# Kernel optimization log

Measured on AMD Instinct MI355X. Metric: run time of the kernel, lower is better.

## Reference

```python
import jax, jax.numpy as jnp
import numpy as np

N, D, F, O = 32768, 32, 128, 128  # nodes, fixed in-degree, in_feats, out_feats


def _lstm_reduce(m, W_ih, W_hh, b_ih, b_hh):
    """Run an LSTM over each node's neighbor mailbox m: [N, T, F] -> final h: [N, H].
    PyTorch gate order: i, f, g, o. W_ih: [4H, F], W_hh: [4H, H]."""
    n, _, _ = m.shape
    H = W_hh.shape[1]
    b = b_ih + b_hh

    def step(carry, x_t):
        h, c = carry
        gates = x_t @ W_ih.T + h @ W_hh.T + b  # [N, 4H]
        i, f, g, o = jnp.split(gates, 4, axis=-1)
        c = jax.nn.sigmoid(f) * c + jax.nn.sigmoid(i) * jnp.tanh(g)
        h = jax.nn.sigmoid(o) * jnp.tanh(c)
        return (h, c), None

    h0 = jnp.zeros((n, H), m.dtype)
    (h_final, _), _ = jax.lax.scan(step, (h0, h0), jnp.swapaxes(m, 0, 1))
    return h_final


def setup_inputs() -> dict:
    key = jax.random.key(0)
    ks = jax.random.split(key, 9)
    stdv_lin = 1.0 / np.sqrt(F)   # linear init: uniform(-1/sqrt(in_feats))
    stdv_lstm = 1.0 / np.sqrt(F)  # torch LSTM init: uniform(-1/sqrt(hidden))
    u = lambda k, shape, s: jax.random.uniform(k, shape, jnp.float32, -s, s)
    return {
        "feat": jax.random.normal(ks[0], (N, F), jnp.float32),
        "neigh_idx": jax.random.randint(ks[1], (N, D), 0, N, jnp.int32),
        "W_ih": u(ks[2], (4 * F, F), stdv_lstm),
        "W_hh": u(ks[3], (4 * F, F), stdv_lstm),
        "b_ih": u(ks[4], (4 * F,), stdv_lstm),
        "b_hh": u(ks[5], (4 * F,), stdv_lstm),
        "W1": u(ks[6], (O, F), stdv_lin),
        "b1": u(ks[6], (O,), stdv_lin),
        "W2": u(ks[7], (O, F), stdv_lin),
        "b2": u(ks[8], (O,), stdv_lin),
    }


def reference(feat, neigh_idx, W_ih, W_hh, b_ih, b_hh, W1, b1, W2, b2):
    # Mailbox gather: each node's D neighbor feature rows -> [N, D, F]
    m = feat[neigh_idx]
    # LSTM reducer -> final hidden state per node
    h = _lstm_reduce(m, W_ih, W_hh, b_ih, b_hh)  # [N, F]
    degs = jnp.asarray(neigh_idx.shape[1], feat.dtype)  # fixed-degree graph
    ah = h / degs
    # feat = linear1(feat) + linear2(ah)
    return feat @ W1.T + b1 + ah @ W2.T + b2
```

## Files before the change

kernel.cpp:

```cpp
#include <hip/hip_runtime.h>
#include <hip/hip_bf16.h>

#define NN 32768
#define DEG 32
#define FF 128
#define OO 128
#define MB 32

typedef __attribute__((ext_vector_type(8))) short bfrag;
typedef __attribute__((ext_vector_type(4))) float f32x4;

#define K1 1.4426950408889634f

__device__ __forceinline__ unsigned short b16(float x) {
    unsigned u = __float_as_uint(x) + 0x8000u;
    return (unsigned short)(u >> 16);
}
__device__ __forceinline__ bfrag pack8(float4 a, float4 b) {
    bfrag r;
    r[0] = (short)b16(a.x); r[1] = (short)b16(a.y); r[2] = (short)b16(a.z); r[3] = (short)b16(a.w);
    r[4] = (short)b16(b.x); r[5] = (short)b16(b.y); r[6] = (short)b16(b.z); r[7] = (short)b16(b.w);
    return r;
}

__device__ __forceinline__ float fsig(float x) {
    return __builtin_amdgcn_rcpf(1.0f + __builtin_amdgcn_exp2f(-K1 * x));
}
__device__ __forceinline__ float ftanh(float x) {
    return fmaf(-2.0f, __builtin_amdgcn_rcpf(1.0f + __builtin_amdgcn_exp2f(2.0f * K1 * x)), 1.0f);
}

__global__ void prep_weights(const float* __restrict__ wih, const float* __restrict__ whh,
                             const float* __restrict__ b_ih, const float* __restrict__ b_hh,
                             const float* __restrict__ w1, const float* __restrict__ b1,
                             const float* __restrict__ w2, const float* __restrict__ b2,
                             short* __restrict__ wihb, short* __restrict__ whhb,
                             short* __restrict__ w1b, short* __restrict__ w2b,
                             float* __restrict__ biasg, float* __restrict__ biaso)
{
    int i = blockIdx.x * blockDim.x + threadIdx.x;
    if (i < 512 * 128) { wihb[i] = (short)b16(wih[i]); whhb[i] = (short)b16(whh[i]); }
    if (i < 128 * 128) { w1b[i] = (short)b16(w1[i]); w2b[i] = (short)b16(w2[i] * 0.03125f); }
    if (i < 512) biasg[i] = b_ih[i] + b_hh[i];
    if (i < 128) biaso[i] = b1[i] + b2[i];
}

__global__ void prep_feat(const float* __restrict__ f, short* __restrict__ fb) {
    int i = blockIdx.x * blockDim.x + threadIdx.x;
    const float4* p = reinterpret_cast<const float4*>(f) + (size_t)i * 2;
    float4 a = p[0], b = p[1];
    *reinterpret_cast<bfrag*>(fb + (size_t)i * 8) = pack8(a, b);
}

template<bool BF16F>
__device__ __forceinline__ bfrag load_row8(const float* __restrict__ ff, const short* __restrict__ fb,
                                           int node, int cs) {
    if (BF16F) {
        return *reinterpret_cast<const bfrag*>(fb + node * FF + cs * 8);
    } else {
        const float4* p = reinterpret_cast<const float4*>(ff + node * FF + cs * 8);
        return pack8(p[0], p[1]);
    }
}

template<bool BF16F>
__global__ __launch_bounds__(512, 2)
void sage_lstm_kernel(const float* __restrict__ featf, const short* __restrict__ featb,
                      const int* __restrict__ nidx,
                      const short* __restrict__ wihb, const short* __restrict__ whhb,
                      const short* __restrict__ w1b, const short* __restrict__ w2b,
                      const float* __restrict__ biasg, const float* __restrict__ biaso,
                      float* __restrict__ out)
{
    __shared__ short xbuf[2][MB * 128];
    __shared__ short hbuf[2][MB * 128];
    __shared__ int   idx_s[MB * DEG];

    const int tid  = (int)threadIdx.x;
    const int lane = tid & 63;
    const int wave = tid >> 6;
    const int n0   = (int)blockIdx.x * MB;

    const int srow = tid >> 4;
    const int cs   = tid & 15;

    idx_s[tid]       = nidx[n0 * DEG + tid];
    idx_s[512 + tid] = nidx[n0 * DEG + 512 + tid];
    {   bfrag z; for (int j = 0; j < 8; ++j) z[j] = 0;
        reinterpret_cast<bfrag*>(hbuf[0])[tid] = z; }

    const int colw = wave * 16 + (lane & 15);
    bfrag wih[4][4], whh[4][4];
#pragma unroll
    for (int g = 0; g < 4; ++g) {
        const short* pih = wihb + (g * 128 + colw) * FF + (lane >> 4) * 8;
        const short* phh = whhb + (g * 128 + colw) * FF + (lane >> 4) * 8;
#pragma unroll
        for (int kt = 0; kt < 4; ++kt) {
            wih[g][kt] = *reinterpret_cast<const bfrag*>(pih + kt * 32);
            whh[g][kt] = *reinterpret_cast<const bfrag*>(phh + kt * 32);
        }
    }
    const float bi = biasg[colw];
    const float bf = biasg[128 + colw];
    const float bg = biasg[256 + colw];
    const float bo = biasg[384 + colw];
    const f32x4 bvi = {bi, bi, bi, bi};
    const f32x4 bvf = {bf, bf, bf, bf};
    const f32x4 bvg = {bg, bg, bg, bg};
    const f32x4 bvo = {bo, bo, bo, bo};

    __syncthreads();

    {
        bfrag v = load_row8<BF16F>(featf, featb, idx_s[srow * DEG], cs);
        int sb = (srow * 256 + cs * 16) ^ ((srow & 7) << 4);
        *reinterpret_cast<bfrag*>(reinterpret_cast<char*>(xbuf[0]) + sb) = v;
    }
    __syncthreads();

    const int arow = lane & 15;
    const int asub = (lane >> 4) * 16;
    const int hr0  = (lane >> 4) * 4;
    const int swz  = (arow & 7) << 4;

    f32x4 p0i, p0f, p0g, p0o, p1i, p1f, p1g, p1o;
    {
        char* x0p = reinterpret_cast<char*>(xbuf[0]);
        bfrag xa[4];
#pragma unroll
        for (int kt = 0; kt < 4; ++kt)
            xa[kt] = *reinterpret_cast<const bfrag*>(x0p + ((arow * 256 + kt * 64 + asub) ^ swz));
        p0i = bvi; p0f = bvf; p0g = bvg; p0o = bvo;
#pragma unroll
        for (int kt = 0; kt < 4; ++kt) {
            p0i = __builtin_amdgcn_mfma_f32_16x16x32_bf16(xa[kt], wih[0][kt], p0i, 0, 0, 0);
            p0f = __builtin_amdgcn_mfma_f32_16x16x32_bf16(xa[kt], wih[1][kt], p0f, 0, 0, 0);
            p0g = __builtin_amdgcn_mfma_f32_16x16x32_bf16(xa[kt], wih[2][kt], p0g, 0, 0, 0);
            p0o = __builtin_amdgcn_mfma_f32_16x16x32_bf16(xa[kt], wih[3][kt], p0o, 0, 0, 0);
        }
#pragma unroll
        for (int kt = 0; kt < 4; ++kt)
            xa[kt] = *reinterpret_cast<const bfrag*>(x0p + (((16 + arow) * 256 + kt * 64 + asub) ^ swz));
        p1i = bvi; p1f = bvf; p1g = bvg; p1o = bvo;
#pragma unroll
        for (int kt = 0; kt < 4; ++kt) {
            p1i = __builtin_amdgcn_mfma_f32_16x16x32_bf16(xa[kt], wih[0][kt], p1i, 0, 0, 0);
            p1f = __builtin_amdgcn_mfma_f32_16x16x32_bf16(xa[kt], wih[1][kt], p1f, 0, 0, 0);
            p1g = __builtin_amdgcn_mfma_f32_16x16x32_bf16(xa[kt], wih[2][kt], p1g, 0, 0, 0);
            p1o = __builtin_amdgcn_mfma_f32_16x16x32_bf16(xa[kt], wih[3][kt], p1o, 0, 0, 0);
        }
    }
    {
        bfrag v = load_row8<BF16F>(featf, featb, idx_s[srow * DEG + 1], cs);
        int sb = (srow * 256 + cs * 16) ^ ((srow & 7) << 4);
        *reinterpret_cast<bfrag*>(reinterpret_cast<char*>(xbuf[1]) + sb) = v;
    }
    __syncthreads();

    f32x4 cs0 = {0.f, 0.f, 0.f, 0.f};
    f32x4 cs1 = {0.f, 0.f, 0.f, 0.f};

#pragma unroll 2
    for (int t = 0; t < DEG; ++t) {
        const int cur = t & 1;
        char* hcur = reinterpret_cast<char*>(hbuf[cur]);
        char* hnxt = reinterpret_cast<char*>(hbuf[cur ^ 1]);
        char* xrd  = reinterpret_cast<char*>(xbuf[cur ^ 1]);
        char* xwr  = reinterpret_cast<char*>(xbuf[cur]);

        bfrag pre2;
        if (t < DEG - 2) pre2 = load_row8<BF16F>(featf, featb, idx_s[srow * DEG + t + 2], cs);

        {
            bfrag ha[4];
#pragma unroll
            for (int kt = 0; kt < 4; ++kt)
                ha[kt] = *reinterpret_cast<const bfrag*>(hcur + ((arow * 256 + kt * 64 + asub) ^ swz));
            f32x4 gi = p0i, gf = p0f, gg = p0g, go = p0o;
#pragma unroll
            for (int kt = 0; kt < 4; ++kt) {
                gi = __builtin_amdgcn_mfma_f32_16x16x32_bf16(ha[kt], whh[0][kt], gi, 0, 0, 0);
                gf = __builtin_amdgcn_mfma_f32_16x16x32_bf16(ha[kt], whh[1][kt], gf, 0, 0, 0);
                gg = __builtin_amdgcn_mfma_f32_16x16x32_bf16(ha[kt], whh[2][kt], gg, 0, 0, 0);
                go = __builtin_amdgcn_mfma_f32_16x16x32_bf16(ha[kt], whh[3][kt], go, 0, 0, 0);
            }
            if (t < DEG - 1) {
                bfrag xn[4];
#pragma unroll
                for (int kt = 0; kt < 4; ++kt)
                    xn[kt] = *reinterpret_cast<const bfrag*>(xrd + ((arow * 256 + kt * 64 + asub) ^ swz));
                p0i = bvi; p0f = bvf; p0g = bvg; p0o = bvo;
#pragma unroll
                for (int kt = 0; kt < 4; ++kt) {
                    p0i = __builtin_amdgcn_mfma_f32_16x16x32_bf16(xn[kt], wih[0][kt], p0i, 0, 0, 0);
                    p0f = __builtin_amdgcn_mfma_f32_16x16x32_bf16(xn[kt], wih[1][kt], p0f, 0, 0, 0);
                    p0g = __builtin_amdgcn_mfma_f32_16x16x32_bf16(xn[kt], wih[2][kt], p0g, 0, 0, 0);
                    p0o = __builtin_amdgcn_mfma_f32_16x16x32_bf16(xn[kt], wih[3][kt], p0o, 0, 0, 0);
                }
            }
#pragma unroll
            for (int r = 0; r < 4; ++r) {
                float iv = fsig(gi[r]);
                float fv = fsig(gf[r]);
                float gv = ftanh(gg[r]);
                float ov = fsig(go[r]);
                float c  = fmaf(fv, cs0[r], iv * gv);
                cs0[r] = c;
                float h  = ov * ftanh(c);
                int hrow = hr0 + r;
                int hb   = (hrow * 256 + colw * 2) ^ ((hrow & 7) << 4);
                *reinterpret_cast<unsigned short*>(hnxt + hb) = b16(h);
            }
        }
        {
            bfrag ha[4];
#pragma unroll
            for (int kt = 0; kt < 4; ++kt)
                ha[kt] = *reinterpret_cast<const bfrag*>(hcur + (((16 + arow) * 256 + kt * 64 + asub) ^ swz));
            f32x4 gi = p1i, gf = p1f, gg = p1g, go = p1o;
#pragma unroll
            for (int kt = 0; kt < 4; ++kt) {
                gi = __builtin_amdgcn_mfma_f32_16x16x32_bf16(ha[kt], whh[0][kt], gi, 0, 0, 0);
                gf = __builtin_amdgcn_mfma_f32_16x16x32_bf16(ha[kt], whh[1][kt], gf, 0, 0, 0);
                gg = __builtin_amdgcn_mfma_f32_16x16x32_bf16(ha[kt], whh[2][kt], gg, 0, 0, 0);
                go = __builtin_amdgcn_mfma_f32_16x16x32_bf16(ha[kt], whh[3][kt], go, 0, 0, 0);
            }
            if (t < DEG - 1) {
                bfrag xn[4];
#pragma unroll
                for (int kt = 0; kt < 4; ++kt)
                    xn[kt] = *reinterpret_cast<const bfrag*>(xrd + (((16 + arow) * 256 + kt * 64 + asub) ^ swz));
                p1i = bvi; p1f = bvf; p1g = bvg; p1o = bvo;
#pragma unroll
                for (int kt = 0; kt < 4; ++kt) {
                    p1i = __builtin_amdgcn_mfma_f32_16x16x32_bf16(xn[kt], wih[0][kt], p1i, 0, 0, 0);
                    p1f = __builtin_amdgcn_mfma_f32_16x16x32_bf16(xn[kt], wih[1][kt], p1f, 0, 0, 0);
                    p1g = __builtin_amdgcn_mfma_f32_16x16x32_bf16(xn[kt], wih[2][kt], p1g, 0, 0, 0);
                    p1o = __builtin_amdgcn_mfma_f32_16x16x32_bf16(xn[kt], wih[3][kt], p1o, 0, 0, 0);
                }
            }
#pragma unroll
            for (int r = 0; r < 4; ++r) {
                float iv = fsig(gi[r]);
                float fv = fsig(gf[r]);
                float gv = ftanh(gg[r]);
                float ov = fsig(go[r]);
                float c  = fmaf(fv, cs1[r], iv * gv);
                cs1[r] = c;
                float h  = ov * ftanh(c);
                int hrow = 16 + hr0 + r;
                int hb   = (hrow * 256 + colw * 2) ^ ((hrow & 7) << 4);
                *reinterpret_cast<unsigned short*>(hnxt + hb) = b16(h);
            }
        }

        if (t < DEG - 2) {
            int sb = (srow * 256 + cs * 16) ^ ((srow & 7) << 4);
            *reinterpret_cast<bfrag*>(xwr + sb) = pre2;
        }
        __syncthreads();
    }

    {
        bfrag v = load_row8<BF16F>(featf, featb, n0 + srow, cs);
        int sb = (srow * 256 + cs * 16) ^ ((srow & 7) << 4);
        *reinterpret_cast<bfrag*>(reinterpret_cast<char*>(xbuf[0]) + sb) = v;
    }
    __syncthreads();

    bfrag w1f[4], w2f[4];
#pragma unroll
    for (int kt = 0; kt < 4; ++kt) {
        w1f[kt] = *reinterpret_cast<const bfrag*>(w1b + colw * FF + kt * 32 + (lane >> 4) * 8);
        w2f[kt] = *reinterpret_cast<const bfrag*>(w2b + colw * FF + kt * 32 + (lane >> 4) * 8);
    }
    const float bb = biaso[colw];
#pragma unroll
    for (int rt = 0; rt < 2; ++rt) {
        const int rowr = rt * 16 + arow;
        bfrag fa[4], hfa[4];
#pragma unroll
        for (int kt = 0; kt < 4; ++kt) {
            int byte = (rowr * 256 + kt * 64 + asub) ^ swz;
            fa[kt]  = *reinterpret_cast<const bfrag*>(reinterpret_cast<char*>(xbuf[0]) + byte);
            hfa[kt] = *reinterpret_cast<const bfrag*>(reinterpret_cast<char*>(hbuf[0]) + byte);
        }
        f32x4 acc = {0.f, 0.f, 0.f, 0.f};
#pragma unroll
        for (int kt = 0; kt < 4; ++kt) {
            acc = __builtin_amdgcn_mfma_f32_16x16x32_bf16(fa[kt],  w1f[kt], acc, 0, 0, 0);
            acc = __builtin_amdgcn_mfma_f32_16x16x32_bf16(hfa[kt], w2f[kt], acc, 0, 0, 0);
        }
#pragma unroll
        for (int r = 0; r < 4; ++r) {
            int orow = n0 + rt * 16 + hr0 + r;
            out[orow * OO + colw] = acc[r] + bb;
        }
    }
}

extern "C" void kernel_launch(void* const* d_in, const int* in_sizes, int n_in,
                              void* d_out, int out_size, void* d_ws, size_t ws_size,
                              hipStream_t stream)
{
    const float* feat = (const float*)d_in[0];
    const int*   nidx = (const int*)d_in[1];
    const float* W_ih = (const float*)d_in[2];
    const float* W_hh = (const float*)d_in[3];
    const float* b_ih = (const float*)d_in[4];
    const float* b_hh = (const float*)d_in[5];
    const float* W1   = (const float*)d_in[6];
    const float* b1   = (const float*)d_in[7];
    const float* W2   = (const float*)d_in[8];
    const float* b2   = (const float*)d_in[9];
    float* out = (float*)d_out;

    char* ws = (char*)d_ws;
    short* wihb  = (short*)(ws);
    short* whhb  = (short*)(ws + 131072);
    short* w1b   = (short*)(ws + 262144);
    short* w2b   = (short*)(ws + 294912);
    float* biasg = (float*)(ws + 327680);
    float* biaso = (float*)(ws + 329728);
    short* featb = (short*)(ws + 330240);

    const size_t need = 330240 + (size_t)NN * FF * 2;
    const bool bf = ws_size >= need;

    prep_weights<<<256, 256, 0, stream>>>(W_ih, W_hh, b_ih, b_hh, W1, b1, W2, b2,
                                          wihb, whhb, w1b, w2b, biasg, biaso);
    if (bf) {
        prep_feat<<<2048, 256, 0, stream>>>(feat, featb);
        sage_lstm_kernel<true><<<NN / MB, 512, 0, stream>>>(feat, featb, nidx, wihb, whhb,
                                                            w1b, w2b, biasg, biaso, out);
    } else {
        sage_lstm_kernel<false><<<NN / MB, 512, 0, stream>>>(feat, featb, nidx, wihb, whhb,
                                                             w1b, w2b, biasg, biaso, out);
    }
}
```

Before: 305.9 us.

## Precompute input projection per node once and gather projected gates in LSTM

Since x_t is a gathered row of feat, the input projection feat@W_ih^T+b is computed once per node (N×512 bf16) in a separate GEMM kernel. The LSTM kernel then gathers these precomputed gate rows via global_load_lds instead of redoing the W_ih MFMA for every neighbour step. This cuts per-step MFMA work roughly in half but quadruples the gathered bytes per neighbour (512 vs 128 bf16). The activation math is also fused to use fewer reciprocals, and the scratch buffer needs more workspace, falling back otherwise.

```diff
diff --git a/kernel.cpp b/kernel.cpp
--- a/kernel.cpp
+++ b/kernel.cpp
@@ -7,14 +7,24 @@
 #define OO 128
 #define MB 32
 
+#define K1 1.4426950408889634f
+#define K2 2.8853900817779268f
+
+#define PPITCH 1056
+#define P0OFF 0
+#define P1OFF 33792
+#define H0OFF 67584
+#define H1OFF 75776
+
 typedef __attribute__((ext_vector_type(8))) short bfrag;
 typedef __attribute__((ext_vector_type(4))) float f32x4;
-
-#define K1 1.4426950408889634f
 
 __device__ __forceinline__ unsigned short b16(float x) {
     unsigned u = __float_as_uint(x) + 0x8000u;
     return (unsigned short)(u >> 16);
+}
+__device__ __forceinline__ float bf2f(unsigned short u) {
+    return __uint_as_float((unsigned)u << 16);
 }
 __device__ __forceinline__ bfrag pack8(float4 a, float4 b) {
     bfrag r;
@@ -22,12 +32,10 @@
     r[4] = (short)b16(b.x); r[5] = (short)b16(b.y); r[6] = (short)b16(b.z); r[7] = (short)b16(b.w);
     return r;
 }
-
-__device__ __forceinline__ float fsig(float x) {
-    return __builtin_amdgcn_rcpf(1.0f + __builtin_amdgcn_exp2f(-K1 * x));
-}
-__device__ __forceinline__ float ftanh(float x) {
-    return fmaf(-2.0f, __builtin_amdgcn_rcpf(1.0f + __builtin_amdgcn_exp2f(2.0f * K1 * x)), 1.0f);
+__device__ __forceinline__ void gload16(const void* g, void* l) {
+    __builtin_amdgcn_global_load_lds(
+        (const __attribute__((address_space(1))) unsigned int*)g,
+        (__attribute__((address_space(3))) unsigned int*)l, 16, 0, 0);
 }
 
 __global__ void prep_weights(const float* __restrict__ wih, const float* __restrict__ whh,
@@ -45,32 +53,217 @@
     if (i < 128) biaso[i] = b1[i] + b2[i];
 }
 
-__global__ void prep_feat(const float* __restrict__ f, short* __restrict__ fb) {
-    int i = blockIdx.x * blockDim.x + threadIdx.x;
-    const float4* p = reinterpret_cast<const float4*>(f) + (size_t)i * 2;
-    float4 a = p[0], b = p[1];
-    *reinterpret_cast<bfrag*>(fb + (size_t)i * 8) = pack8(a, b);
-}
-
-template<bool BF16F>
-__device__ __forceinline__ bfrag load_row8(const float* __restrict__ ff, const short* __restrict__ fb,
-                                           int node, int cs) {
-    if (BF16F) {
-        return *reinterpret_cast<const bfrag*>(fb + node * FF + cs * 8);
-    } else {
-        const float4* p = reinterpret_cast<const float4*>(ff + node * FF + cs * 8);
-        return pack8(p[0], p[1]);
-    }
-}
-
-template<bool BF16F>
 __global__ __launch_bounds__(512, 2)
-void sage_lstm_kernel(const float* __restrict__ featf, const short* __restrict__ featb,
-                      const int* __restrict__ nidx,
-                      const short* __restrict__ wihb, const short* __restrict__ whhb,
-                      const short* __restrict__ w1b, const short* __restrict__ w2b,
-                      const float* __restrict__ biasg, const float* __restrict__ biaso,
-                      float* __restrict__ out)
+void xp_gemm(const float* __restrict__ feat, const short* __restrict__ wihb,
+             const float* __restrict__ biasg, unsigned short* __restrict__ xp)
+{
+    __shared__ short xt[MB * 128];
+
+    const int tid  = (int)threadIdx.x;
+    const int lane = tid & 63;
+    const int wave = tid >> 6;
+    const int n0   = (int)blockIdx.x * MB;
+    const int srow = tid >> 4;
+    const int cs   = tid & 15;
+
+    {   const float4* p = reinterpret_cast<const float4*>(feat + (n0 + srow) * FF + cs * 8);
+        int sb = (srow * 256 + cs * 16) ^ ((srow & 7) << 4);
+        *reinterpret_cast<bfrag*>(reinterpret_cast<char*>(xt) + sb) = pack8(p[0], p[1]); }
+
+    const int colw = wave * 16 + (lane & 15);
+    bfrag wih[4][4];
+#pragma unroll
+    for (int g = 0; g < 4; ++g) {
+        const short* pih = wihb + (g * 128 + colw) * FF + (lane >> 4) * 8;
+#pragma unroll
+        for (int kt = 0; kt < 4; ++kt)
+            wih[g][kt] = *reinterpret_cast<const bfrag*>(pih + kt * 32);
+    }
+    float bg4[4];
+#pragma unroll
+    for (int g = 0; g < 4; ++g) bg4[g] = biasg[g * 128 + colw];
+
+    __syncthreads();
+
+    const int arow = lane & 15;
+    const int asub = (lane >> 4) * 16;
+    const int hr0  = (lane >> 4) * 4;
+    const int swz  = (arow & 7) << 4;
+    const char* xtp = reinterpret_cast<const char*>(xt);
+
+#pragma unroll
+    for (int rt = 0; rt < 2; ++rt) {
+        bfrag a[4];
+#pragma unroll
+        for (int kt = 0; kt < 4; ++kt)
+            a[kt] = *reinterpret_cast<const bfrag*>(xtp + (((rt * 16 + arow) * 256 + kt * 64 + asub) ^ swz));
+#pragma unroll
+        for (int g = 0; g < 4; ++g) {
+            f32x4 acc = {bg4[g], bg4[g], bg4[g], bg4[g]};
+#pragma unroll
+            for (int kt = 0; kt < 4; ++kt)
+                acc = __builtin_amdgcn_mfma_f32_16x16x32_bf16(a[kt], wih[g][kt], acc, 0, 0, 0);
+#pragma unroll
+            for (int r = 0; r < 4; ++r)
+                xp[(n0 + rt * 16 + hr0 + r) * 512 + g * 128 + colw] = b16(acc[r]);
+        }
+    }
+}
+
+__global__ __launch_bounds__(512, 2)
+void sage_xp(const float* __restrict__ feat, const int* __restrict__ nidx,
+             const unsigned short* __restrict__ xp,
+             const short* __restrict__ whhb, const short* __restrict__ w1b,
+             const short* __restrict__ w2b, const float* __restrict__ biaso,
+             float* __restrict__ out)
+{
+    __shared__ char lds[83968];
+    __shared__ int  idx_s[MB * DEG];
+
+    const int tid  = (int)threadIdx.x;
+    const int lane = tid & 63;
+    const int wave = tid >> 6;
+    const int n0   = (int)blockIdx.x * MB;
+    const int srow = tid >> 4;
+    const int cs   = tid & 15;
+
+    idx_s[tid]       = nidx[n0 * DEG + tid];
+    idx_s[512 + tid] = nidx[n0 * DEG + 512 + tid];
+    {   bfrag z = {0, 0, 0, 0, 0, 0, 0, 0};
+        *reinterpret_cast<bfrag*>(lds + H0OFF + tid * 16) = z; }
+
+    const int colw = wave * 16 + (lane & 15);
+    bfrag whh[4][4];
+#pragma unroll
+    for (int g = 0; g < 4; ++g) {
+        const short* phh = whhb + (g * 128 + colw) * FF + (lane >> 4) * 8;
+#pragma unroll
+        for (int kt = 0; kt < 4; ++kt)
+            whh[g][kt] = *reinterpret_cast<const bfrag*>(phh + kt * 32);
+    }
+    __syncthreads();
+
+#pragma unroll
+    for (int j = 0; j < 4; ++j) {
+        int nd = idx_s[(wave * 4 + j) * DEG + 0];
+        gload16(xp + nd * 512 + lane * 8, lds + P0OFF + (wave * 4 + j) * PPITCH);
+    }
+    __syncthreads();
+
+    const int arow = lane & 15;
+    const int asub = (lane >> 4) * 16;
+    const int hr0  = (lane >> 4) * 4;
+    const int swz  = (arow & 7) << 4;
+
+    f32x4 cs0 = {0.f, 0.f, 0.f, 0.f};
+    f32x4 cs1 = {0.f, 0.f, 0.f, 0.f};
+
+    auto rdP = [&](const char* pc, int goff) {
+        f32x4 v;
+        v[0] = bf2f(*reinterpret_cast<const unsigned short*>(pc + goff));
+        v[1] = bf2f(*reinterpret_cast<const unsigned short*>(pc + goff + PPITCH));
+        v[2] = bf2f(*reinterpret_cast<const unsigned short*>(pc + goff + 2 * PPITCH));
+        v[3] = bf2f(*reinterpret_cast<const unsigned short*>(pc + goff + 3 * PPITCH));
+        return v;
+    };
+
+    auto dort = [&](int rt, int pcur, int hcur, int hnxt, f32x4& cst) {
+        bfrag ha[4];
+#pragma unroll
+        for (int kt = 0; kt < 4; ++kt)
+            ha[kt] = *reinterpret_cast<const bfrag*>(
+                lds + hcur + (((rt * 16 + arow) * 256 + kt * 64 + asub) ^ swz));
+        const char* pc = lds + pcur + (rt * 16 + hr0) * PPITCH + colw * 2;
+        f32x4 gi = rdP(pc, 0), gf = rdP(pc, 256), gg = rdP(pc, 512), go = rdP(pc, 768);
+#pragma unroll
+        for (int kt = 0; kt < 4; ++kt) {
+            gi = __builtin_amdgcn_mfma_f32_16x16x32_bf16(ha[kt], whh[0][kt], gi, 0, 0, 0);
+            gf = __builtin_amdgcn_mfma_f32_16x16x32_bf16(ha[kt], whh[1][kt], gf, 0, 0, 0);
+            gg = __builtin_amdgcn_mfma_f32_16x16x32_bf16(ha[kt], whh[2][kt], gg, 0, 0, 0);
+            go = __builtin_amdgcn_mfma_f32_16x16x32_bf16(ha[kt], whh[3][kt], go, 0, 0, 0);
+        }
+#pragma unroll
+        for (int r = 0; r < 4; ++r) {
+            float av = __builtin_amdgcn_exp2f(-K1 * gi[r]);
+            float bv = __builtin_amdgcn_exp2f(K2 * fminf(gg[r], 40.0f));
+            float dv = __builtin_amdgcn_exp2f(-K1 * gf[r]);
+            float ev = __builtin_amdgcn_exp2f(-K1 * go[r]);
+            float t1 = __builtin_amdgcn_rcpf((1.0f + av) * (1.0f + bv));
+            float t2 = __builtin_amdgcn_rcpf(1.0f + dv);
+            float c  = fmaf(cst[r], t2, (bv - 1.0f) * t1);
+            cst[r] = c;
+            float uv = __builtin_amdgcn_exp2f(K2 * c);
+            float t3 = __builtin_amdgcn_rcpf((1.0f + ev) * (1.0f + uv));
+            float h  = (uv - 1.0f) * t3;
+            int hrow = rt * 16 + hr0 + r;
+            int hb   = (hrow * 256 + colw * 2) ^ ((hrow & 7) << 4);
+            *reinterpret_cast<unsigned short*>(lds + hnxt + hb) = b16(h);
+        }
+    };
+
+#define STEP(T, PCUR, PNXT, HCUR, HNXT)                                         \
+    {                                                                           \
+        if ((T) < DEG - 1) {                                                    \
+            _Pragma("unroll")                                                   \
+            for (int j = 0; j < 4; ++j) {                                       \
+                int nd = idx_s[(wave * 4 + j) * DEG + (T) + 1];                 \
+                gload16(xp + nd * 512 + lane * 8,                               \
+                        lds + (PNXT) + (wave * 4 + j) * PPITCH);                \
+            }                                                                   \
+        }                                                                       \
+        dort(0, PCUR, HCUR, HNXT, cs0);                                         \
+        dort(1, PCUR, HCUR, HNXT, cs1);                                         \
+        __syncthreads();                                                        \
+    }
+
+#pragma unroll 1
+    for (int tt = 0; tt < DEG; tt += 2) {
+        STEP(tt,     P0OFF, P1OFF, H0OFF, H1OFF);
+        STEP(tt + 1, P1OFF, P0OFF, H1OFF, H0OFF);
+    }
+#undef STEP
+
+    {   const float4* p = reinterpret_cast<const float4*>(feat + (n0 + srow) * FF + cs * 8);
+        int sb = (srow * 256 + cs * 16) ^ ((srow & 7) << 4);
+        *reinterpret_cast<bfrag*>(lds + P0OFF + sb) = pack8(p[0], p[1]); }
+    __syncthreads();
+
+    bfrag w1f[4], w2f[4];
+#pragma unroll
+    for (int kt = 0; kt < 4; ++kt) {
+        w1f[kt] = *reinterpret_cast<const bfrag*>(w1b + colw * FF + kt * 32 + (lane >> 4) * 8);
+        w2f[kt] = *reinterpret_cast<const bfrag*>(w2b + colw * FF + kt * 32 + (lane >> 4) * 8);
+    }
+    const float bb = biaso[colw];
+#pragma unroll
+    for (int rt = 0; rt < 2; ++rt) {
+        bfrag fa[4], hfa[4];
+#pragma unroll
+        for (int kt = 0; kt < 4; ++kt) {
+            int byte = ((rt * 16 + arow) * 256 + kt * 64 + asub) ^ swz;
+            fa[kt]  = *reinterpret_cast<const bfrag*>(lds + P0OFF + byte);
+            hfa[kt] = *reinterpret_cast<const bfrag*>(lds + H0OFF + byte);
+        }
+        f32x4 acc = {0.f, 0.f, 0.f, 0.f};
+#pragma unroll
+        for (int kt = 0; kt < 4; ++kt) {
+            acc = __builtin_amdgcn_mfma_f32_16x16x32_bf16(fa[kt],  w1f[kt], acc, 0, 0, 0);
+            acc = __builtin_amdgcn_mfma_f32_16x16x32_bf16(hfa[kt], w2f[kt], acc, 0, 0, 0);
+        }
+#pragma unroll
+        for (int r = 0; r < 4; ++r) {
+            int orow = n0 + rt * 16 + hr0 + r;
+            out[orow * OO + colw] = acc[r] + bb;
+        }
+    }
+}
+
+__global__ __launch_bounds__(512, 2)
+void sage_lstm_fb(const float* __restrict__ featf, const int* __restrict__ nidx,
+                  const short* __restrict__ wihb, const short* __restrict__ whhb,
+                  const short* __restrict__ w1b, const short* __restrict__ w2b,
+                  const float* __restrict__ biasg, const float* __restrict__ biaso,
+                  float* __restrict__ out)
 {
     __shared__ short xbuf[2][MB * 128];
     __shared__ short hbuf[2][MB * 128];
@@ -80,13 +273,12 @@
     const int lane = tid & 63;
     const int wave = tid >> 6;
     const int n0   = (int)blockIdx.x * MB;
-
     const int srow = tid >> 4;
     const int cs   = tid & 15;
 
     idx_s[tid]       = nidx[n0 * DEG + tid];
     idx_s[512 + tid] = nidx[n0 * DEG + 512 + tid];
-    {   bfrag z; for (int j = 0; j < 8; ++j) z[j] = 0;
+    {   bfrag z = {0, 0, 0, 0, 0, 0, 0, 0};
         reinterpret_cast<bfrag*>(hbuf[0])[tid] = z; }
 
     const int colw = wave * 16 + (lane & 15);
@@ -111,11 +303,10 @@
     const f32x4 bvo = {bo, bo, bo, bo};
 
     __syncthreads();
-
     {
-        bfrag v = load_row8<BF16F>(featf, featb, idx_s[srow * DEG], cs);
+        const float4* p = reinterpret_cast<const float4*>(featf + idx_s[srow * DEG] * FF + cs * 8);
         int sb = (srow * 256 + cs * 16) ^ ((srow & 7) << 4);
-        *reinterpret_cast<bfrag*>(reinterpret_cast<char*>(xbuf[0]) + sb) = v;
+        *reinterpret_cast<bfrag*>(reinterpret_cast<char*>(xbuf[0]) + sb) = pack8(p[0], p[1]);
     }
     __syncthreads();
 
@@ -124,42 +315,58 @@
     const int hr0  = (lane >> 4) * 4;
     const int swz  = (arow & 7) << 4;
 
+    auto mm4 = [&](const char* p, int rbase, const bfrag (&W)[4][4],
+                   f32x4& vi, f32x4& vf, f32x4& vg, f32x4& vo) {
+        bfrag a[4];
+#pragma unroll
+        for (int kt = 0; kt < 4; ++kt)
+            a[kt] = *reinterpret_cast<const bfrag*>(p + ((rbase * 256 + kt * 64 + asub) ^ swz));
+#pragma unroll
+        for (int kt = 0; kt < 4; ++kt) {
+            vi = __builtin_amdgcn_mfma_f32_16x16x32_bf16(a[kt], W[0][kt], vi, 0, 0, 0);
+            vf = __builtin_amdgcn_mfma_f32_16x16x32_bf16(a[kt], W[1][kt], vf, 0, 0, 0);
+            vg = __builtin_amdgcn_mfma_f32_16x16x32_bf16(a[kt], W[2][kt], vg, 0, 0, 0);
+            vo = __builtin_amdgcn_mfma_f32_16x16x32_bf16(a[kt], W[3][kt], vo, 0, 0, 0);
+        }
+    };
+    auto actw = [&](f32x4& gi, f32x4& gf, f32x4& gg, f32x4& go,
+                    f32x4& cst, char* hnxt, int rt) {
+#pragma unroll
+        for (int r = 0; r < 4; ++r) {
+            float av = __builtin_amdgcn_exp2f(-K1 * gi[r]);
+            float bv = __builtin_amdgcn_exp2f(K2 * fminf(gg[r], 40.0f));
+            float dv = __builtin_amdgcn_exp2f(-K1 * gf[r]);
+            float ev = __builtin_amdgcn_exp2f(-K1 * go[r]);
+            float t1 = __builtin_amdgcn_rcpf((1.0f + av) * (1.0f + bv));
+            float t2 = __builtin_amdgcn_rcpf(1.0f + dv);
+            float c  = fmaf(cst[r], t2, (bv - 1.0f) * t1);
+            cst[r] = c;
+            float uv = __builtin_amdgcn_exp2f(K2 * c);
+            float t3 = __builtin_amdgcn_rcpf((1.0f + ev) * (1.0f + uv));
+            float h  = (uv - 1.0f) * t3;
+            int hrow = rt * 16 + hr0 + r;
+            int hb   = (hrow * 256 + colw * 2) ^ ((hrow & 7) << 4);
+            *reinterpret_cast<unsigned short*>(hnxt + hb) = b16(h);
+        }
+    };
+
     f32x4 p0i, p0f, p0g, p0o, p1i, p1f, p1g, p1o;
     {
         char* x0p = reinterpret_cast<char*>(xbuf[0]);
-        bfrag xa[4];
-#pragma unroll
-        for (int kt = 0; kt < 4; ++kt)
-            xa[kt] = *reinterpret_cast<const bfrag*>(x0p + ((arow * 256 + kt * 64 + asub) ^ swz));
         p0i = bvi; p0f = bvf; p0g = bvg; p0o = bvo;
-#pragma unroll
-        for (int kt = 0; kt < 4; ++kt) {
-            p0i = __builtin_amdgcn_mfma_f32_16x16x32_bf16(xa[kt], wih[0][kt], p0i, 0, 0, 0);
-            p0f = __builtin_amdgcn_mfma_f32_16x16x32_bf16(xa[kt], wih[1][kt], p0f, 0, 0, 0);
-            p0g = __builtin_amdgcn_mfma_f32_16x16x32_bf16(xa[kt], wih[2][kt], p0g, 0, 0, 0);
-            p0o = __builtin_amdgcn_mfma_f32_16x16x32_bf16(xa[kt], wih[3][kt], p0o, 0, 0, 0);
-        }
-#pragma unroll
-        for (int kt = 0; kt < 4; ++kt)
-            xa[kt] = *reinterpret_cast<const bfrag*>(x0p + (((16 + arow) * 256 + kt * 64 + asub) ^ swz));
+        mm4(x0p, arow, wih, p0i, p0f, p0g, p0o);
         p1i = bvi; p1f = bvf; p1g = bvg; p1o = bvo;
-#pragma unroll
-        for (int kt = 0; kt < 4; ++kt) {
-            p1i = __builtin_amdgcn_mfma_f32_16x16x32_bf16(xa[kt], wih[0][kt], p1i, 0, 0, 0);
-            p1f = __builtin_amdgcn_mfma_f32_16x16x32_bf16(xa[kt], wih[1][kt], p1f, 0, 0, 0);
-            p1g = __builtin_amdgcn_mfma_f32_16x16x32_bf16(xa[kt], wih[2][kt], p1g, 0, 0, 0);
-            p1o = __builtin_amdgcn_mfma_f32_16x16x32_bf16(xa[kt], wih[3][kt], p1o, 0, 0, 0);
-        }
+        mm4(x0p, 16 + arow, wih, p1i, p1f, p1g, p1o);
     }
     {
-        bfrag v = load_row8<BF16F>(featf, featb, idx_s[srow * DEG + 1], cs);
+        const float4* p = reinterpret_cast<const float4*>(featf + idx_s[srow * DEG + 1] * FF + cs * 8);
         int sb = (srow * 256 + cs * 16) ^ ((srow & 7) << 4);
-        *reinterpret_cast<bfrag*>(reinterpret_cast<char*>(xbuf[1]) + sb) = v;
-    }
-    __syncthreads();
-
-    f32x4 cs0 = {0.f, 0.f, 0.f, 0.f};
-    f32x4 cs1 = {0.f, 0.f, 0.f, 0.f};
+        *reinterpret_cast<bfrag*>(reinterpret_cast<char*>(xbuf[1]) + sb) = pack8(p[0], p[1]);
+    }
+    __syncthreads();
+
+    const f32x4 zz = {0.f, 0.f, 0.f, 0.f};
+    f32x4 cs0 = zz, cs1 = zz;
 
 #pragma unroll 2
     for (int t = 0; t < DEG; ++t) {
@@ -170,91 +377,28 @@
         char* xwr  = reinterpret_cast<char*>(xbuf[cur]);
 
         bfrag pre2;
-        if (t < DEG - 2) pre2 = load_row8<BF16F>(featf, featb, idx_s[srow * DEG + t + 2], cs);
-
+        if (t < DEG - 2) {
+            const float4* p = reinterpret_cast<const float4*>(featf + idx_s[srow * DEG + t + 2] * FF + cs * 8);
+            pre2 = pack8(p[0], p[1]);
+        }
         {
-            bfrag ha[4];
-#pragma unroll
-            for (int kt = 0; kt < 4; ++kt)
-                ha[kt] = *reinterpret_cast<const bfrag*>(hcur + ((arow * 256 + kt * 64 + asub) ^ swz));
             f32x4 gi = p0i, gf = p0f, gg = p0g, go = p0o;
-#pragma unroll
-            for (int kt = 0; kt < 4; ++kt) {
-                gi = __builtin_amdgcn_mfma_f32_16x16x32_bf16(ha[kt], whh[0][kt], gi, 0, 0, 0);
-                gf = __builtin_amdgcn_mfma_f32_16x16x32_bf16(ha[kt], whh[1][kt], gf, 0, 0, 0);
-                gg = __builtin_amdgcn_mfma_f32_16x16x32_bf16(ha[kt], whh[2][kt], gg, 0, 0, 0);
-                go = __builtin_amdgcn_mfma_f32_16x16x32_bf16(ha[kt], whh[3][kt], go, 0, 0, 0);
+            mm4(hcur, arow, whh, gi, gf, gg, go);
+            if (t < DEG - 1) {
+                p0i = bvi; p0f = bvf; p0g = bvg; p0o = bvo;
+                mm4(xrd, arow, wih, p0i, p0f, p0g, p0o);
             }
+            actw(gi, gf, gg, go, cs0, hnxt, 0);
+        }
+        {
+            f32x4 gi = p1i, gf = p1f, gg = p1g, go = p1o;
+            mm4(hcur, 16 + arow, whh, gi, gf, gg, go);
             if (t < DEG - 1) {
-                bfrag xn[4];
-#pragma unroll
-                for (int kt = 0; kt < 4; ++kt)
-                    xn[kt] = *reinterpret_cast<const bfrag*>(xrd + ((arow * 256 + kt * 64 + asub) ^ swz));
-                p0i = bvi; p0f = bvf; p0g = bvg; p0o = bvo;
-#pragma unroll
-                for (int kt = 0; kt < 4; ++kt) {
-                    p0i = __builtin_amdgcn_mfma_f32_16x16x32_bf16(xn[kt], wih[0][kt], p0i, 0, 0, 0);
-                    p0f = __builtin_amdgcn_mfma_f32_16x16x32_bf16(xn[kt], wih[1][kt], p0f, 0, 0, 0);
-                    p0g = __builtin_amdgcn_mfma_f32_16x16x32_bf16(xn[kt], wih[2][kt], p0g, 0, 0, 0);
-                    p0o = __builtin_amdgcn_mfma_f32_16x16x32_bf16(xn[kt], wih[3][kt], p0o, 0, 0, 0);
-                }
+                p1i = bvi; p1f = bvf; p1g = bvg; p1o = bvo;
+                mm4(xrd, 16 + arow, wih, p1i, p1f, p1g, p1o);
             }
-#pragma unroll
-            for (int r = 0; r < 4; ++r) {
-                float iv = fsig(gi[r]);
-                float fv = fsig(gf[r]);
-                float gv = ftanh(gg[r]);
-                float ov = fsig(go[r]);
-                float c  = fmaf(fv, cs0[r], iv * gv);
-                cs0[r] = c;
-                float h  = ov * ftanh(c);
-                int hrow = hr0 + r;
-                int hb   = (hrow * 256 + colw * 2) ^ ((hrow & 7) << 4);
-                *reinterpret_cast<unsigned short*>(hnxt + hb) = b16(h);
-            }
-        }
-        {
-            bfrag ha[4];
-#pragma unroll
-            for (int kt = 0; kt < 4; ++kt)
-                ha[kt] = *reinterpret_cast<const bfrag*>(hcur + (((16 + arow) * 256 + kt * 64 + asub) ^ swz));
-            f32x4 gi = p1i, gf = p1f, gg = p1g, go = p1o;
-#pragma unroll
-            for (int kt = 0; kt < 4; ++kt) {
-                gi = __builtin_amdgcn_mfma_f32_16x16x32_bf16(ha[kt], whh[0][kt], gi, 0, 0, 0);
-                gf = __builtin_amdgcn_mfma_f32_16x16x32_bf16(ha[kt], whh[1][kt], gf, 0, 0, 0);
-                gg = __builtin_amdgcn_mfma_f32_16x16x32_bf16(ha[kt], whh[2][kt], gg, 0, 0, 0);
-                go = __builtin_amdgcn_mfma_f32_16x16x32_bf16(ha[kt], whh[3][kt], go, 0, 0, 0);
-            }
-            if (t < DEG - 1) {
-                bfrag xn[4];
-#pragma unroll
-                for (int kt = 0; kt < 4; ++kt)
-                    xn[kt] = *reinterpret_cast<const bfrag*>(xrd + (((16 + arow) * 256 + kt * 64 + asub) ^ swz));
-                p1i = bvi; p1f = bvf; p1g = bvg; p1o = bvo;
-#pragma unroll
-                for (int kt = 0; kt < 4; ++kt) {
-                    p1i = __builtin_amdgcn_mfma_f32_16x16x32_bf16(xn[kt], wih[0][kt], p1i, 0, 0, 0);
-                    p1f = __builtin_amdgcn_mfma_f32_16x16x32_bf16(xn[kt], wih[1][kt], p1f, 0, 0, 0);
-                    p1g = __builtin_amdgcn_mfma_f32_16x16x32_bf16(xn[kt], wih[2][kt], p1g, 0, 0, 0);
-                    p1o = __builtin_amdgcn_mfma_f32_16x16x32_bf16(xn[kt], wih[3][kt], p1o, 0, 0, 0);
-                }
-            }
-#pragma unroll
-            for (int r = 0; r < 4; ++r) {
-                float iv = fsig(gi[r]);
-                float fv = fsig(gf[r]);
-                float gv = ftanh(gg[r]);
-                float ov = fsig(go[r]);
-                float c  = fmaf(fv, cs1[r], iv * gv);
-                cs1[r] = c;
-                float h  = ov * ftanh(c);
-                int hrow = 16 + hr0 + r;
-                int hb   = (hrow * 256 + colw * 2) ^ ((hrow & 7) << 4);
-                *reinterpret_cast<unsigned short*>(hnxt + hb) = b16(h);
-            }
-        }
-
+            actw(gi, gf, gg, go, cs1, hnxt, 1);
+        }
         if (t < DEG - 2) {
             int sb = (srow * 256 + cs * 16) ^ ((srow & 7) << 4);
             *reinterpret_cast<bfrag*>(xwr + sb) = pre2;
@@ -263,12 +407,14 @@
     }
 
     {
-        bfrag v = load_row8<BF16F>(featf, featb, n0 + srow, cs);
+        const float4* p = reinterpret_cast<const float4*>(featf + (n0 + srow) * FF + cs * 8);
         int sb = (srow * 256 + cs * 16) ^ ((srow & 7) << 4);
-        *reinterpret_cast<bfrag*>(reinterpret_cast<char*>(xbuf[0]) + sb) = v;
-    }
-    __syncthreads();
-
+        *reinterpret_cast<bfrag*>(reinterpret_cast<char*>(xbuf[0]) + sb) = pack8(p[0], p[1]);
+    }
+    __syncthreads();
+
+    char* const x0p = reinterpret_cast<char*>(xbuf[0]);
+    char* const h0p = reinterpret_cast<char*>(hbuf[0]);
     bfrag w1f[4], w2f[4];
 #pragma unroll
     for (int kt = 0; kt < 4; ++kt) {
@@ -278,13 +424,12 @@
     const float bb = biaso[colw];
 #pragma unroll
     for (int rt = 0; rt < 2; ++rt) {
-        const int rowr = rt * 16 + arow;
         bfrag fa[4], hfa[4];
 #pragma unroll
         for (int kt = 0; kt < 4; ++kt) {
-            int byte = (rowr * 256 + kt * 64 + asub) ^ swz;
-            fa[kt]  = *reinterpret_cast<const bfrag*>(reinterpret_cast<char*>(xbuf[0]) + byte);
-            hfa[kt] = *reinterpret_cast<const bfrag*>(reinterpret_cast<char*>(hbuf[0]) + byte);
+            int byte = ((rt * 16 + arow) * 256 + kt * 64 + asub) ^ swz;
+            fa[kt]  = *reinterpret_cast<const bfrag*>(x0p + byte);
+            hfa[kt] = *reinterpret_cast<const bfrag*>(h0p + byte);
         }
         f32x4 acc = {0.f, 0.f, 0.f, 0.f};
 #pragma unroll
@@ -323,19 +468,17 @@
     short* w2b   = (short*)(ws + 294912);
     float* biasg = (float*)(ws + 327680);
     float* biaso = (float*)(ws + 329728);
-    short* featb = (short*)(ws + 330240);
-
-    const size_t need = 330240 + (size_t)NN * FF * 2;
-    const bool bf = ws_size >= need;
+    unsigned short* xpb = (unsigned short*)(ws + 330240);
+
+    const size_t need = 330240 + (size_t)NN * 512 * 2;
 
     prep_weights<<<256, 256, 0, stream>>>(W_ih, W_hh, b_ih, b_hh, W1, b1, W2, b2,
                                           wihb, whhb, w1b, w2b, biasg, biaso);
-    if (bf) {
-        prep_feat<<<2048, 256, 0, stream>>>(feat, featb);
-        sage_lstm_kernel<true><<<NN / MB, 512, 0, stream>>>(feat, featb, nidx, wihb, whhb,
-                                                            w1b, w2b, biasg, biaso, out);
+    if (ws_size >= need) {
+        xp_gemm<<<NN / MB, 512, 0, stream>>>(feat, wihb, biasg, xpb);
+        sage_xp<<<NN / MB, 512, 0, stream>>>(feat, nidx, xpb, whhb, w1b, w2b, biaso, out);
     } else {
-        sage_lstm_kernel<false><<<NN / MB, 512, 0, stream>>>(feat, featb, nidx, wihb, whhb,
-                                                             w1b, w2b, biasg, biaso, out);
-    }
-}
+        sage_lstm_fb<<<NN / MB, 512, 0, stream>>>(feat, nidx, wihb, whhb,
+                                                  w1b, w2b, biasg, biaso, out);
+    }
+}
```

Result: slower. 359.4 us (+17.5%).
